# Kernel optimization log

Measured on AMD Instinct MI355X. Metric: run time of the kernel, lower is better.

## Reference

```python
import jax, jax.numpy as jnp
import numpy as np

B, T, D = 8, 1024, 1024
H, HS = 16, 64  # num_heads, head_size; H*HS == D


def setup_inputs() -> dict:
    key = jax.random.key(0)
    ks = jax.random.split(key, 5)
    scale = 0.02
    x = jax.random.normal(ks[0], (B, T, D), dtype=jnp.float32)
    Wq = jax.random.normal(ks[1], (H, D, HS), dtype=jnp.float32) * scale
    Wk = jax.random.normal(ks[2], (H, D, HS), dtype=jnp.float32) * scale
    Wv = jax.random.normal(ks[3], (H, D, HS), dtype=jnp.float32) * scale
    Wo = jax.random.normal(ks[4], (D, D), dtype=jnp.float32) * scale
    bo = jnp.zeros((D,), dtype=jnp.float32)
    return {"x": x, "Wq": Wq, "Wk": Wk, "Wv": Wv, "Wo": Wo, "bo": bo}


def reference(x, Wq, Wk, Wv, Wo, bo):
    # Per-head linear projections (bias-free, as in Head): [B,H,T,HS]
    q = jnp.einsum('btd,hds->bhts', x, Wq)
    k = jnp.einsum('btd,hds->bhts', x, Wk)
    v = jnp.einsum('btd,hds->bhts', x, Wv)
    # Scaled scores with causal mask: [B,H,T,T]
    scores = jnp.einsum('bhts,bhus->bhtu', q, k) * (HS ** -0.5)
    causal = jnp.tril(jnp.ones((T, T), dtype=bool))
    scores = jnp.where(causal, scores, jnp.finfo(scores.dtype).min)
    att = jax.nn.softmax(scores, axis=-1)
    # Weighted sum over values, then concat heads: [B,T,H*HS]
    out = jnp.einsum('bhtu,bhus->bhts', att, v)
    out = out.transpose(0, 2, 1, 3).reshape(B, T, H * HS)
    # Output projection (nn.Linear: y = x @ W^T + b)
    return out @ Wo.T + bo
```

## Files before the change

### kernel.cpp

```cpp
#include <hip/hip_runtime.h>
#include <hip/hip_bf16.h>

#define BBATCH 8
#define TSEQ   1024
#define DMODEL 1024
#define NHEAD  16
#define HSZ    64

typedef unsigned short ushort_t;
typedef __attribute__((ext_vector_type(8))) short short8;
typedef __attribute__((ext_vector_type(4))) float float4v;

__device__ __forceinline__ ushort_t f2bf(float f) {
    __hip_bfloat16 h = __float2bfloat16(f);
    return *reinterpret_cast<ushort_t*>(&h);
}
__device__ __forceinline__ ushort_t f2bf_fast(float f) {
    return (ushort_t)((__float_as_uint(f) + 0x8000u) >> 16);
}
__device__ __forceinline__ unsigned int pack_bf2(float lo, float hi) {
    unsigned int a = __float_as_uint(lo) + 0x8000u;
    unsigned int b = __float_as_uint(hi) + 0x8000u;
    return __builtin_amdgcn_perm(b, a, 0x07060302u);
}

__device__ __forceinline__ short8 cvt8(const float* f) {
    union { ushort_t u[8]; short8 v; } r;
    #pragma unroll
    for (int e = 0; e < 8; ++e) r.u[e] = f2bf(f[e]);
    return r.v;
}

__device__ __forceinline__ void async16(const ushort_t* g, ushort_t* l) {
    __builtin_amdgcn_global_load_lds(
        (const __attribute__((address_space(1))) unsigned int*)g,
        (__attribute__((address_space(3))) unsigned int*)l, 16, 0, 0);
}

__global__ __launch_bounds__(256) void cvt_f32_bf16(
    const float* __restrict__ src, ushort_t* __restrict__ dst)
{
    const size_t idx = ((size_t)blockIdx.x * 256 + threadIdx.x) * 16;
    float f[16];
    *(float4*)(f + 0)  = *(const float4*)(src + idx);
    *(float4*)(f + 4)  = *(const float4*)(src + idx + 4);
    *(float4*)(f + 8)  = *(const float4*)(src + idx + 8);
    *(float4*)(f + 12) = *(const float4*)(src + idx + 12);
    uint4 o0 = make_uint4(pack_bf2(f[0], f[1]),   pack_bf2(f[2], f[3]),
                          pack_bf2(f[4], f[5]),   pack_bf2(f[6], f[7]));
    uint4 o1 = make_uint4(pack_bf2(f[8], f[9]),   pack_bf2(f[10], f[11]),
                          pack_bf2(f[12], f[13]), pack_bf2(f[14], f[15]));
    *(uint4*)(dst + idx) = o0;
    *(uint4*)(dst + idx + 8) = o1;
}

__global__ __launch_bounds__(256) void pack_w(
    const float* __restrict__ Wq, const float* __restrict__ Wk,
    const float* __restrict__ Wv, ushort_t* __restrict__ WpT)
{
    __shared__ ushort_t L[64 * 72];
    const int tid = threadIdx.x;
    const int d0 = blockIdx.x * 64;
    const int wh = blockIdx.y;
    const int w = wh >> 4, h = wh & 15;
    const float* W = (w == 0 ? Wq : (w == 1 ? Wk : Wv)) + (size_t)h * DMODEL * HSZ;

    int dr = tid >> 2, sc = (tid & 3) * 16;
    const float4* src = (const float4*)(W + (size_t)(d0 + dr) * HSZ + sc);
    float f[16];
    *(float4*)(f + 0) = src[0]; *(float4*)(f + 4) = src[1];
    *(float4*)(f + 8) = src[2]; *(float4*)(f + 12) = src[3];
    *(short8*)(L + dr * 72 + sc)     = cvt8(f);
    *(short8*)(L + dr * 72 + sc + 8) = cvt8(f + 8);
    __syncthreads();

    int s = tid >> 2, dc = (tid & 3) * 16;
    union { ushort_t u[16]; short8 v[2]; } o;
    #pragma unroll
    for (int j = 0; j < 16; ++j) o.u[j] = L[(dc + j) * 72 + s];
    ushort_t* dst = WpT + (size_t)(w * 1024 + h * 64 + s) * DMODEL + d0 + dc;
    *(short8*)dst = o.v[0];
    *(short8*)(dst + 8) = o.v[1];
}

__global__ __launch_bounds__(256) void transpose_v(
    const ushort_t* __restrict__ Vb, ushort_t* __restrict__ Vt)
{
    __shared__ ushort_t L[64 * 72];
    const int tid = threadIdx.x;
    const int t0 = blockIdx.x * 64;
    const int bh = blockIdx.y;
    const size_t base = (size_t)bh * TSEQ * HSZ;

    int r = tid >> 2, c16 = (tid & 3) * 16;
    const ushort_t* src = Vb + base + (size_t)(t0 + r) * HSZ + c16;
    *(short8*)(L + r * 72 + c16)     = *(const short8*)src;
    *(short8*)(L + r * 72 + c16 + 8) = *(const short8*)(src + 8);
    __syncthreads();

    int s = tid >> 2, tc = (tid & 3) * 16;
    union { ushort_t u[16]; short8 v[2]; } o;
    #pragma unroll
    for (int j = 0; j < 16; ++j) o.u[j] = L[(tc + j) * 72 + s];
    ushort_t* dst = Vt + base + (size_t)s * TSEQ + t0 + tc;
    *(short8*)dst = o.v[0];
    *(short8*)(dst + 8) = o.v[1];
}

__global__ __launch_bounds__(256) void qkv_gemm(
    const ushort_t* __restrict__ Xb, const ushort_t* __restrict__ WpT,
    ushort_t* __restrict__ Qb, ushort_t* __restrict__ Kb, ushort_t* __restrict__ Vb)
{
    __shared__ ushort_t As[128 * 64];
    __shared__ ushort_t Bs[128 * 64];
    const int tid = threadIdx.x;
    const int wave = tid >> 6, lane = tid & 63;
    const int q = lane >> 4, cc = lane & 15;
    const int bid = blockIdx.x;
    const int n_blk = (bid & 7) + 8 * (bid >> 9);
    const int m_blk = (bid >> 3) & 63;
    const int n0 = n_blk * 128, m0 = m_blk * 128;
    const int wm = wave >> 1, wn = wave & 1;

    const ushort_t* ag[4]; const ushort_t* bg[4]; int lo_[4];
    #pragma unroll
    for (int i = 0; i < 4; ++i) {
        int row = wave * 32 + i * 8 + (lane >> 3);
        int ch = (lane & 7) ^ (row & 7);
        ag[i] = Xb + (size_t)(m0 + row) * DMODEL + ch * 8;
        bg[i] = WpT + (size_t)(n0 + row) * DMODEL + ch * 8;
        lo_[i] = (wave * 32 + i * 8) * 64;
    }
    int aoff[4][2], boff[4][2];
    #pragma unroll
    for (int mt = 0; mt < 4; ++mt) {
        int row = wm * 64 + mt * 16 + cc;
        #pragma unroll
        for (int kt = 0; kt < 2; ++kt)
            aoff[mt][kt] = row * 64 + (((kt * 4 + q) ^ (row & 7)) * 8);
    }
    #pragma unroll
    for (int nt = 0; nt < 4; ++nt) {
        int row = wn * 64 + nt * 16 + cc;
        #pragma unroll
        for (int kt = 0; kt < 2; ++kt)
            boff[nt][kt] = row * 64 + (((kt * 4 + q) ^ (row & 7)) * 8);
    }

    float4v acc[4][4];
    #pragma unroll
    for (int a = 0; a < 4; ++a)
        #pragma unroll
        for (int b = 0; b < 4; ++b) acc[a][b] = (float4v){0.f, 0.f, 0.f, 0.f};

    for (int j = 0; j < 16; ++j) {
        #pragma unroll
        for (int i = 0; i < 4; ++i) {
            async16(ag[i], As + lo_[i]);
            async16(bg[i], Bs + lo_[i]);
            ag[i] += 64; bg[i] += 64;
        }
        __syncthreads();

        short8 av[4][2], bv[4][2];
        #pragma unroll
        for (int mt = 0; mt < 4; ++mt) {
            av[mt][0] = *(const short8*)(As + aoff[mt][0]);
            av[mt][1] = *(const short8*)(As + aoff[mt][1]);
        }
        #pragma unroll
        for (int nt = 0; nt < 4; ++nt) {
            bv[nt][0] = *(const short8*)(Bs + boff[nt][0]);
            bv[nt][1] = *(const short8*)(Bs + boff[nt][1]);
        }
        #pragma unroll
        for (int kt = 0; kt < 2; ++kt)
            #pragma unroll
            for (int mt = 0; mt < 4; ++mt)
                #pragma unroll
                for (int nt = 0; nt < 4; ++nt)
                    acc[mt][nt] = __builtin_amdgcn_mfma_f32_16x16x32_bf16(
                        av[mt][kt], bv[nt][kt], acc[mt][nt], 0, 0, 0);
        __syncthreads();
    }

    const int nbase = n0 + wn * 64;
    const int wsel = nbase >> 10;
    const int h = (nbase >> 6) & 15;
    ushort_t* Out = wsel == 0 ? Qb : (wsel == 1 ? Kb : Vb);
    const float osc = (wsel == 0) ? 0.18033688011112042f : 1.0f;
    #pragma unroll
    for (int mt = 0; mt < 4; ++mt)
        #pragma unroll
        for (int rr = 0; rr < 4; ++rr) {
            int m = m0 + wm * 64 + mt * 16 + q * 4 + rr;
            int b = m >> 10, t = m & 1023;
            size_t rb = (((size_t)(b * NHEAD + h)) * TSEQ + t) * HSZ;
            #pragma unroll
            for (int nt = 0; nt < 4; ++nt)
                Out[rb + nt * 16 + cc] = f2bf_fast(acc[mt][nt][rr] * osc);
        }
}

__global__ __launch_bounds__(256) void attn(
    const ushort_t* __restrict__ Qb, const ushort_t* __restrict__ Kb,
    const ushort_t* __restrict__ Vt, ushort_t* __restrict__ Ob)
{
    __shared__ ushort_t Ks[2][64 * 64];
    __shared__ ushort_t VTs[2][64 * 64];
    __shared__ ushort_t Ps[4][32 * 72];
    const int tid = threadIdx.x;
    const int wave = tid >> 6, lane = tid & 63;
    const int q = lane >> 4, cc = lane & 15;
    const int bid = blockIdx.x;
    const int qt = 7 - (bid >> 7);
    const int bh = bid & 127;
    const size_t base = (size_t)bh * TSEQ * HSZ;
    const int J = 2 * qt + 2;

    const ushort_t* kg[2]; const ushort_t* vg[2]; int dmo[2];
    #pragma unroll
    for (int i = 0; i < 2; ++i) {
        int rr = wave * 16 + i * 8 + (lane >> 3);
        int ch = (lane & 7) ^ (rr & 7);
        kg[i] = Kb + base + (size_t)rr * HSZ + ch * 8;
        vg[i] = Vt + base + (size_t)rr * TSEQ + ch * 8;
        dmo[i] = (wave * 16 + i * 8) * 64;
    }

    short8 qf[2][2];
    #pragma unroll
    for (int tt = 0; tt < 2; ++tt) {
        const ushort_t* qp = Qb + base +
            (size_t)(qt * 128 + wave * 32 + tt * 16 + cc) * HSZ + q * 8;
        qf[tt][0] = *(const short8*)qp;
        qf[tt][1] = *(const short8*)(qp + 32);
    }

    int koff[4][2], poff[2][2];
    #pragma unroll
    for (int ut = 0; ut < 4; ++ut)
        #pragma unroll
        for (int kt = 0; kt < 2; ++kt)
            koff[ut][kt] = (ut * 16 + cc) * 64 + (((kt * 4 + q) ^ (cc & 7)) * 8);
    #pragma unroll
    for (int tt = 0; tt < 2; ++tt)
        #pragma unroll
        for (int kt = 0; kt < 2; ++kt)
            poff[tt][kt] = (tt * 16 + cc) * 72 + kt * 32 + q * 8;

    float4v oacc[2][4];
    #pragma unroll
    for (int tt = 0; tt < 2; ++tt)
        #pragma unroll
        for (int st = 0; st < 4; ++st) oacc[tt][st] = (float4v){0.f, 0.f, 0.f, 0.f};
    float lsum[2] = {0.f, 0.f};

    #pragma unroll
    for (int i = 0; i < 2; ++i) {
        async16(kg[i], &Ks[0][dmo[i]]);
        async16(vg[i], &VTs[0][dmo[i]]);
    }
    __syncthreads();

    for (int jt = 0; jt < J; ++jt) {
        const ushort_t* Kc = Ks[jt & 1];
        const ushort_t* Vc = VTs[jt & 1];
        if (jt + 1 < J) {
            int nb = (jt + 1) & 1;
            #pragma unroll
            for (int i = 0; i < 2; ++i) {
                async16(kg[i] + (size_t)(jt + 1) * 64 * HSZ, &Ks[nb][dmo[i]]);
                async16(vg[i] + (jt + 1) * 64, &VTs[nb][dmo[i]]);
            }
        }

        float4v sc[4][2];
        #pragma unroll
        for (int ut = 0; ut < 4; ++ut)
            #pragma unroll
            for (int tt = 0; tt < 2; ++tt) sc[ut][tt] = (float4v){0.f, 0.f, 0.f, 0.f};
        #pragma unroll
        for (int kt = 0; kt < 2; ++kt) {
            short8 kf[4];
            #pragma unroll
            for (int ut = 0; ut < 4; ++ut) kf[ut] = *(const short8*)(Kc + koff[ut][kt]);
            #pragma unroll
            for (int ut = 0; ut < 4; ++ut) {
                sc[ut][0] = __builtin_amdgcn_mfma_f32_16x16x32_bf16(
                    kf[ut], qf[0][kt], sc[ut][0], 0, 0, 0);
                sc[ut][1] = __builtin_amdgcn_mfma_f32_16x16x32_bf16(
                    kf[ut], qf[1][kt], sc[ut][1], 0, 0, 0);
            }
        }

        const bool diag = ((jt >> 1) == qt);
        #pragma unroll
        for (int tt = 0; tt < 2; ++tt) {
            const int tg = qt * 128 + wave * 32 + tt * 16 + cc;
            #pragma unroll
            for (int ut = 0; ut < 4; ++ut) {
                float pv[4]; float ps = 0.f;
                #pragma unroll
                for (int rr = 0; rr < 4; ++rr) {
                    float p = exp2f(sc[ut][tt][rr]);
                    if (diag && (jt * 64 + ut * 16 + q * 4 + rr) > tg) p = 0.f;
                    pv[rr] = p; ps += p;
                }
                lsum[tt] += ps;
                *(uint2*)&Ps[wave][(tt * 16 + cc) * 72 + ut * 16 + q * 4] =
                    make_uint2(pack_bf2(pv[0], pv[1]), pack_bf2(pv[2], pv[3]));
            }
        }

        #pragma unroll
        for (int kt = 0; kt < 2; ++kt) {
            short8 pa0 = *(const short8*)&Ps[wave][poff[0][kt]];
            short8 pa1 = *(const short8*)&Ps[wave][poff[1][kt]];
            #pragma unroll
            for (int st = 0; st < 4; ++st) {
                short8 vf = *(const short8*)(Vc + koff[st][kt]);
                oacc[0][st] = __builtin_amdgcn_mfma_f32_16x16x32_bf16(
                    pa0, vf, oacc[0][st], 0, 0, 0);
                oacc[1][st] = __builtin_amdgcn_mfma_f32_16x16x32_bf16(
                    pa1, vf, oacc[1][st], 0, 0, 0);
            }
        }
        __syncthreads();
    }

    float inv[2];
    #pragma unroll
    for (int tt = 0; tt < 2; ++tt) {
        float l = lsum[tt];
        l += __shfl_xor(l, 16);
        l += __shfl_xor(l, 32);
        inv[tt] = 1.f / l;
    }
    const int b = bh >> 4, h = bh & 15;
    #pragma unroll
    for (int tt = 0; tt < 2; ++tt)
        #pragma unroll
        for (int rr = 0; rr < 4; ++rr) {
            float iv = __shfl(inv[tt], q * 4 + rr);
            int t = qt * 128 + wave * 32 + tt * 16 + q * 4 + rr;
            size_t rb = ((size_t)b * TSEQ + t) * DMODEL + h * HSZ;
            #pragma unroll
            for (int st = 0; st < 4; ++st)
                Ob[rb + st * 16 + cc] = f2bf_fast(oacc[tt][st][rr] * iv);
        }
}

__global__ __launch_bounds__(256) void oproj_gemm(
    const ushort_t* __restrict__ Obuf, const ushort_t* __restrict__ Wob,
    const float* __restrict__ bo, float* __restrict__ out)
{
    __shared__ ushort_t As[128 * 64];
    __shared__ ushort_t Bs[128 * 64];
    const int tid = threadIdx.x;
    const int wave = tid >> 6, lane = tid & 63;
    const int q = lane >> 4, cc = lane & 15;
    const int bid = blockIdx.x;
    const int n0 = (bid & 7) * 128, m0 = (bid >> 3) * 128;
    const int wm = wave >> 1, wn = wave & 1;

    const ushort_t* ag[4]; const ushort_t* bg[4]; int lo_[4];
    #pragma unroll
    for (int i = 0; i < 4; ++i) {
        int row = wave * 32 + i * 8 + (lane >> 3);
        int ch = (lane & 7) ^ (row & 7);
        ag[i] = Obuf + (size_t)(m0 + row) * DMODEL + ch * 8;
        bg[i] = Wob + (size_t)(n0 + row) * DMODEL + ch * 8;
        lo_[i] = (wave * 32 + i * 8) * 64;
    }
    int aoff[4][2], boff[4][2];
    #pragma unroll
    for (int mt = 0; mt < 4; ++mt) {
        int row = wm * 64 + mt * 16 + cc;
        #pragma unroll
        for (int kt = 0; kt < 2; ++kt)
            aoff[mt][kt] = row * 64 + (((kt * 4 + q) ^ (row & 7)) * 8);
    }
    #pragma unroll
    for (int nt = 0; nt < 4; ++nt) {
        int row = wn * 64 + nt * 16 + cc;
        #pragma unroll
        for (int kt = 0; kt < 2; ++kt)
            boff[nt][kt] = row * 64 + (((kt * 4 + q) ^ (row & 7)) * 8);
    }

    float4v acc[4][4];
    #pragma unroll
    for (int a = 0; a < 4; ++a)
        #pragma unroll
        for (int b = 0; b < 4; ++b) acc[a][b] = (float4v){0.f, 0.f, 0.f, 0.f};

    for (int j = 0; j < 16; ++j) {
        #pragma unroll
        for (int i = 0; i < 4; ++i) {
            async16(ag[i], As + lo_[i]);
            async16(bg[i], Bs + lo_[i]);
            ag[i] += 64; bg[i] += 64;
        }
        __syncthreads();

        short8 av[4][2], bv[4][2];
        #pragma unroll
        for (int mt = 0; mt < 4; ++mt) {
            av[mt][0] = *(const short8*)(As + aoff[mt][0]);
            av[mt][1] = *(const short8*)(As + aoff[mt][1]);
        }
        #pragma unroll
        for (int nt = 0; nt < 4; ++nt) {
            bv[nt][0] = *(const short8*)(Bs + boff[nt][0]);
            bv[nt][1] = *(const short8*)(Bs + boff[nt][1]);
        }
        #pragma unroll
        for (int kt = 0; kt < 2; ++kt)
            #pragma unroll
            for (int mt = 0; mt < 4; ++mt)
                #pragma unroll
                for (int nt = 0; nt < 4; ++nt)
                    acc[mt][nt] = __builtin_amdgcn_mfma_f32_16x16x32_bf16(
                        av[mt][kt], bv[nt][kt], acc[mt][nt], 0, 0, 0);
        __syncthreads();
    }

    #pragma unroll
    for (int nt = 0; nt < 4; ++nt) {
        int n = n0 + wn * 64 + nt * 16 + cc;
        float bias = bo[n];
        #pragma unroll
        for (int mt = 0; mt < 4; ++mt)
            #pragma unroll
            for (int rr = 0; rr < 4; ++rr) {
                int m = m0 + wm * 64 + mt * 16 + q * 4 + rr;
                out[(size_t)m * DMODEL + n] = acc[mt][nt][rr] + bias;
            }
    }
}

extern "C" void kernel_launch(void* const* d_in, const int* in_sizes, int n_in,
                              void* d_out, int out_size, void* d_ws, size_t ws_size,
                              hipStream_t stream)
{
    const float* x  = (const float*)d_in[0];
    const float* Wq = (const float*)d_in[1];
    const float* Wk = (const float*)d_in[2];
    const float* Wv = (const float*)d_in[3];
    const float* Wo = (const float*)d_in[4];
    const float* bo = (const float*)d_in[5];
    float* out = (float*)d_out;

    const size_t SEG = (size_t)8 * 1024 * 1024;
    ushort_t* Qb  = (ushort_t*)d_ws;
    ushort_t* Kb  = Qb + SEG;
    ushort_t* Vb  = Kb + SEG;
    ushort_t* Ob  = Vb;
    ushort_t* WpT = Vb + SEG;
    ushort_t* Vtb = WpT;
    ushort_t* Xb  = (ushort_t*)d_out;
    ushort_t* Wob = Kb;

    cvt_f32_bf16<<<dim3(2048),    256, 0, stream>>>(x, Xb);
    pack_w      <<<dim3(16, 48),  256, 0, stream>>>(Wq, Wk, Wv, WpT);
    qkv_gemm    <<<dim3(1536),    256, 0, stream>>>(Xb, WpT, Qb, Kb, Vb);
    transpose_v <<<dim3(16, 128), 256, 0, stream>>>(Vb, Vtb);
    attn        <<<dim3(1024),    256, 0, stream>>>(Qb, Kb, Vtb, Ob);
    cvt_f32_bf16<<<dim3(256),     256, 0, stream>>>(Wo, Wob);
    oproj_gemm  <<<dim3(512),     256, 0, stream>>>(Ob, Wob, bo, out);
}
```

Measured before the change: 247.4 us.

## Fuse V transpose into QKV GEMM epilogue, remap blocks per XCD, split causal mask path

The QKV GEMM now writes V directly in transposed [b,h,s,t] layout with packed 4-element stores, which removes the separate transpose_v kernel and its extra round trip through memory. For Q/K tiles the MFMA operands are swapped so each lane holds four consecutive head-dim values and can issue packed 8-byte stores instead of scalar ones. Block-to-tile mapping in both GEMMs is reordered so that consecutive M tiles land on the same XCD, aiming for better L2 reuse. The attention softmax gets a separate diagonal branch so off-diagonal tiles skip the mask compare. Workspace buffers are reassigned to fit the new layout, which costs extra per-branch code and register pressure.

```diff
diff --git a/kernel.cpp b/kernel.cpp
--- a/kernel.cpp
+++ b/kernel.cpp
@@ -83,33 +83,9 @@
     *(short8*)(dst + 8) = o.v[1];
 }
 
-__global__ __launch_bounds__(256) void transpose_v(
-    const ushort_t* __restrict__ Vb, ushort_t* __restrict__ Vt)
-{
-    __shared__ ushort_t L[64 * 72];
-    const int tid = threadIdx.x;
-    const int t0 = blockIdx.x * 64;
-    const int bh = blockIdx.y;
-    const size_t base = (size_t)bh * TSEQ * HSZ;
-
-    int r = tid >> 2, c16 = (tid & 3) * 16;
-    const ushort_t* src = Vb + base + (size_t)(t0 + r) * HSZ + c16;
-    *(short8*)(L + r * 72 + c16)     = *(const short8*)src;
-    *(short8*)(L + r * 72 + c16 + 8) = *(const short8*)(src + 8);
-    __syncthreads();
-
-    int s = tid >> 2, tc = (tid & 3) * 16;
-    union { ushort_t u[16]; short8 v[2]; } o;
-    #pragma unroll
-    for (int j = 0; j < 16; ++j) o.u[j] = L[(tc + j) * 72 + s];
-    ushort_t* dst = Vt + base + (size_t)s * TSEQ + t0 + tc;
-    *(short8*)dst = o.v[0];
-    *(short8*)(dst + 8) = o.v[1];
-}
-
 __global__ __launch_bounds__(256) void qkv_gemm(
     const ushort_t* __restrict__ Xb, const ushort_t* __restrict__ WpT,
-    ushort_t* __restrict__ Qb, ushort_t* __restrict__ Kb, ushort_t* __restrict__ Vb)
+    ushort_t* __restrict__ Qb, ushort_t* __restrict__ Kb, ushort_t* __restrict__ Vt)
 {
     __shared__ ushort_t As[128 * 64];
     __shared__ ushort_t Bs[128 * 64];
@@ -117,10 +93,12 @@
     const int wave = tid >> 6, lane = tid & 63;
     const int q = lane >> 4, cc = lane & 15;
     const int bid = blockIdx.x;
-    const int n_blk = (bid & 7) + 8 * (bid >> 9);
-    const int m_blk = (bid >> 3) & 63;
+    const int xcd = bid & 7, local = bid >> 3;
+    const int n_blk = local >> 3;
+    const int m_blk = xcd * 8 + (local & 7);
     const int n0 = n_blk * 128, m0 = m_blk * 128;
     const int wm = wave >> 1, wn = wave & 1;
+    const bool isV = (n0 >= 2048);
 
     const ushort_t* ag[4]; const ushort_t* bg[4]; int lo_[4];
     #pragma unroll
@@ -173,33 +151,63 @@
             bv[nt][0] = *(const short8*)(Bs + boff[nt][0]);
             bv[nt][1] = *(const short8*)(Bs + boff[nt][1]);
         }
-        #pragma unroll
-        for (int kt = 0; kt < 2; ++kt)
-            #pragma unroll
-            for (int mt = 0; mt < 4; ++mt)
+        if (isV) {
+            #pragma unroll
+            for (int kt = 0; kt < 2; ++kt)
+                #pragma unroll
+                for (int mt = 0; mt < 4; ++mt)
+                    #pragma unroll
+                    for (int nt = 0; nt < 4; ++nt)
+                        acc[mt][nt] = __builtin_amdgcn_mfma_f32_16x16x32_bf16(
+                            av[mt][kt], bv[nt][kt], acc[mt][nt], 0, 0, 0);
+        } else {
+            #pragma unroll
+            for (int kt = 0; kt < 2; ++kt)
                 #pragma unroll
                 for (int nt = 0; nt < 4; ++nt)
-                    acc[mt][nt] = __builtin_amdgcn_mfma_f32_16x16x32_bf16(
-                        av[mt][kt], bv[nt][kt], acc[mt][nt], 0, 0, 0);
+                    #pragma unroll
+                    for (int mt = 0; mt < 4; ++mt)
+                        acc[nt][mt] = __builtin_amdgcn_mfma_f32_16x16x32_bf16(
+                            bv[nt][kt], av[mt][kt], acc[nt][mt], 0, 0, 0);
+        }
         __syncthreads();
     }
 
-    const int nbase = n0 + wn * 64;
-    const int wsel = nbase >> 10;
-    const int h = (nbase >> 6) & 15;
-    ushort_t* Out = wsel == 0 ? Qb : (wsel == 1 ? Kb : Vb);
-    const float osc = (wsel == 0) ? 0.18033688011112042f : 1.0f;
-    #pragma unroll
-    for (int mt = 0; mt < 4; ++mt)
-        #pragma unroll
-        for (int rr = 0; rr < 4; ++rr) {
-            int m = m0 + wm * 64 + mt * 16 + q * 4 + rr;
-            int b = m >> 10, t = m & 1023;
-            size_t rb = (((size_t)(b * NHEAD + h)) * TSEQ + t) * HSZ;
-            #pragma unroll
-            for (int nt = 0; nt < 4; ++nt)
-                Out[rb + nt * 16 + cc] = f2bf_fast(acc[mt][nt][rr] * osc);
-        }
+    if (isV) {
+        #pragma unroll
+        for (int mt = 0; mt < 4; ++mt) {
+            int m = m0 + wm * 64 + mt * 16 + q * 4;
+            int b = m >> 10, t0_ = m & 1023;
+            #pragma unroll
+            for (int nt = 0; nt < 4; ++nt) {
+                int n = n0 + wn * 64 + nt * 16 + cc;
+                int h = (n >> 6) & 15, s = n & 63;
+                size_t addr = (((size_t)(b * NHEAD + h)) * HSZ + s) * TSEQ + t0_;
+                uint2 pk = make_uint2(pack_bf2(acc[mt][nt][0], acc[mt][nt][1]),
+                                      pack_bf2(acc[mt][nt][2], acc[mt][nt][3]));
+                *(uint2*)(Vt + addr) = pk;
+            }
+        }
+    } else {
+        const int nbase = n0 + wn * 64;
+        ushort_t* Out = (nbase < 1024) ? Qb : Kb;
+        const float osc = (nbase < 1024) ? 0.18033688011112042f : 1.0f;
+        #pragma unroll
+        for (int mt = 0; mt < 4; ++mt) {
+            int m = m0 + wm * 64 + mt * 16 + cc;
+            int b = m >> 10, t_ = m & 1023;
+            #pragma unroll
+            for (int nt = 0; nt < 4; ++nt) {
+                int n = nbase + nt * 16 + q * 4;
+                int h = (n >> 6) & 15, s0 = n & 63;
+                size_t addr = (((size_t)(b * NHEAD + h)) * TSEQ + t_) * HSZ + s0;
+                uint2 pk = make_uint2(
+                    pack_bf2(acc[nt][mt][0] * osc, acc[nt][mt][1] * osc),
+                    pack_bf2(acc[nt][mt][2] * osc, acc[nt][mt][3] * osc));
+                *(uint2*)(Out + addr) = pk;
+            }
+        }
+    }
 }
 
 __global__ __launch_bounds__(256) void attn(
@@ -294,22 +302,39 @@
             }
         }
 
-        const bool diag = ((jt >> 1) == qt);
-        #pragma unroll
-        for (int tt = 0; tt < 2; ++tt) {
-            const int tg = qt * 128 + wave * 32 + tt * 16 + cc;
-            #pragma unroll
-            for (int ut = 0; ut < 4; ++ut) {
-                float pv[4]; float ps = 0.f;
+        if ((jt >> 1) == qt) {
+            #pragma unroll
+            for (int tt = 0; tt < 2; ++tt) {
+                const int tg = qt * 128 + wave * 32 + tt * 16 + cc;
                 #pragma unroll
-                for (int rr = 0; rr < 4; ++rr) {
-                    float p = exp2f(sc[ut][tt][rr]);
-                    if (diag && (jt * 64 + ut * 16 + q * 4 + rr) > tg) p = 0.f;
-                    pv[rr] = p; ps += p;
+                for (int ut = 0; ut < 4; ++ut) {
+                    float pv[4]; float ps = 0.f;
+                    #pragma unroll
+                    for (int rr = 0; rr < 4; ++rr) {
+                        float p = exp2f(sc[ut][tt][rr]);
+                        if ((jt * 64 + ut * 16 + q * 4 + rr) > tg) p = 0.f;
+                        pv[rr] = p; ps += p;
+                    }
+                    lsum[tt] += ps;
+                    *(uint2*)&Ps[wave][(tt * 16 + cc) * 72 + ut * 16 + q * 4] =
+                        make_uint2(pack_bf2(pv[0], pv[1]), pack_bf2(pv[2], pv[3]));
                 }
-                lsum[tt] += ps;
-                *(uint2*)&Ps[wave][(tt * 16 + cc) * 72 + ut * 16 + q * 4] =
-                    make_uint2(pack_bf2(pv[0], pv[1]), pack_bf2(pv[2], pv[3]));
+            }
+        } else {
+            #pragma unroll
+            for (int tt = 0; tt < 2; ++tt) {
+                #pragma unroll
+                for (int ut = 0; ut < 4; ++ut) {
+                    float pv[4]; float ps = 0.f;
+                    #pragma unroll
+                    for (int rr = 0; rr < 4; ++rr) {
+                        float p = exp2f(sc[ut][tt][rr]);
+                        pv[rr] = p; ps += p;
+                    }
+                    lsum[tt] += ps;
+                    *(uint2*)&Ps[wave][(tt * 16 + cc) * 72 + ut * 16 + q * 4] =
+                        make_uint2(pack_bf2(pv[0], pv[1]), pack_bf2(pv[2], pv[3]));
+                }
             }
         }
 
@@ -361,7 +386,9 @@
     const int wave = tid >> 6, lane = tid & 63;
     const int q = lane >> 4, cc = lane & 15;
     const int bid = blockIdx.x;
-    const int n0 = (bid & 7) * 128, m0 = (bid >> 3) * 128;
+    const int xcd = bid & 7, local = bid >> 3;
+    const int n0 = (local >> 3) * 128;
+    const int m0 = (xcd * 8 + (local & 7)) * 128;
     const int wm = wave >> 1, wn = wave & 1;
 
     const ushort_t* ag[4]; const ushort_t* bg[4]; int lo_[4];
@@ -455,17 +482,15 @@
     const size_t SEG = (size_t)8 * 1024 * 1024;
     ushort_t* Qb  = (ushort_t*)d_ws;
     ushort_t* Kb  = Qb + SEG;
-    ushort_t* Vb  = Kb + SEG;
-    ushort_t* Ob  = Vb;
-    ushort_t* WpT = Vb + SEG;
-    ushort_t* Vtb = WpT;
+    ushort_t* Vtb = Kb + SEG;
+    ushort_t* WpT = Vtb + SEG;
+    ushort_t* Ob  = WpT;
     ushort_t* Xb  = (ushort_t*)d_out;
-    ushort_t* Wob = Kb;
+    ushort_t* Wob = Qb;
 
     cvt_f32_bf16<<<dim3(2048),    256, 0, stream>>>(x, Xb);
     pack_w      <<<dim3(16, 48),  256, 0, stream>>>(Wq, Wk, Wv, WpT);
-    qkv_gemm    <<<dim3(1536),    256, 0, stream>>>(Xb, WpT, Qb, Kb, Vb);
-    transpose_v <<<dim3(16, 128), 256, 0, stream>>>(Vb, Vtb);
+    qkv_gemm    <<<dim3(1536),    256, 0, stream>>>(Xb, WpT, Qb, Kb, Vtb);
     attn        <<<dim3(1024),    256, 0, stream>>>(Qb, Kb, Vtb, Ob);
     cvt_f32_bf16<<<dim3(256),     256, 0, stream>>>(Wo, Wob);
     oproj_gemm  <<<dim3(512),     256, 0, stream>>>(Ob, Wob, bo, out);
```

Result: faster. 230.7 us (-6.8%).
